# Optimization experiments

Hardware: AMD Instinct MI355X
Metric: run time of the kernel (lower is better)

Reference implementation:

```python
import jax, jax.numpy as jnp
import numpy as np

B, T, H, K = 2048, 200, 256, 8


def setup_inputs() -> dict:
    key = jax.random.key(0)
    ks = jax.random.split(key, 8)
    s = 1.0 / np.sqrt(H)  # torch nn.Linear default init range
    vm = jax.random.uniform(ks[5], (B, T)) < 0.6
    vm = vm.at[:, :3].set(True)  # guarantee >=3 valid visits so history_mask is non-empty
    return {
        "current_state": jax.random.normal(ks[0], (B, H), jnp.float32),
        "state_sequence": jax.random.normal(ks[1], (B, T, H), jnp.float32),
        "visit_mask": vm,
        "Wq": jax.random.uniform(ks[2], (H, H), jnp.float32, -s, s),
        "bq": jnp.zeros((H,), jnp.float32),
        "Wk": jax.random.uniform(ks[3], (H, H), jnp.float32, -s, s),
        "bk": jnp.zeros((H,), jnp.float32),
        "Wv": jax.random.uniform(ks[4], (H, H), jnp.float32, -s, s),
        "bv": jnp.zeros((H,), jnp.float32),
    }


def reference(current_state, state_sequence, visit_mask, Wq, bq, Wk, bk, Wv, bv):
    mask = visit_mask.astype(bool)
    valid_counts = mask.sum(axis=1)  # (B,)
    t_idx = jnp.arange(T)[None, :]
    # attend only to visits strictly before the last valid one
    history_mask = mask & (t_idx < (valid_counts - 1)[:, None])

    q = current_state @ Wq + bq                      # (B,H)
    k = state_sequence @ Wk + bk                     # (B,T,H)
    v = jax.nn.relu(state_sequence @ Wv + bv)        # dropout is identity in eval

    scores = jnp.einsum('bth,bh->bt', k, q) / np.sqrt(H).astype(np.float32)
    scores = jnp.where(history_mask, scores, -1e9)
    attn = jax.nn.softmax(scores, axis=-1)
    attn = jnp.where(history_mask, attn, 0.0)
    norm = attn.sum(-1, keepdims=True)
    attn = attn / jnp.where(norm > 0, norm, 1.0)

    # vectorized per-row top-K sparsify + renormalize (replaces the python loop)
    masked = jnp.where(history_mask, attn, -1.0)
    vals, idx = jax.lax.top_k(masked, K)             # (B,K)
    keep_vals = jnp.maximum(vals, 0.0)               # invalid slots had -1 -> contribute 0
    sparse = jnp.zeros_like(attn).at[jnp.arange(B)[:, None], idx].set(keep_vals)
    eps = jnp.finfo(attn.dtype).eps
    attn = sparse / jnp.maximum(sparse.sum(-1, keepdims=True), eps)

    summary = jnp.einsum('bth,bt->bh', v, attn)
    has_history = history_mask.any(axis=1, keepdims=True)
    summary = jnp.where(has_history, summary, 0.0)

    # selected visit indices (top-K of final weights, -1 where outside history)
    _, midx = jax.lax.top_k(jnp.where(history_mask, attn, -1.0), K)
    sel_mask = jnp.take_along_axis(history_mask, midx, axis=1)
    selected = jnp.where(sel_mask, midx, -1).astype(jnp.int32)

    return summary, attn, selected
```

## Files before the change

### kernel.cpp

```cpp
#include <hip/hip_runtime.h>
#include <cstddef>

#define BB 2048
#define TT 200
#define HH 256
#define KK 8

#define WS_M2T  0
#define WS_EVEC 65792
#define WS_F    66048

__device__ __forceinline__ float wred_sum(float v) {
#pragma unroll
  for (int off = 32; off; off >>= 1) v += __shfl_xor(v, off);
  return v;
}
__device__ __forceinline__ float wred_max(float v) {
#pragma unroll
  for (int off = 32; off; off >>= 1) v = fmaxf(v, __shfl_xor(v, off));
  return v;
}

__global__ __launch_bounds__(256) void prep_all(
    const float* __restrict__ Wq, const float* __restrict__ bq,
    const float* __restrict__ Wk, const float* __restrict__ bk,
    float* __restrict__ M2T, float* __restrict__ evec, float* __restrict__ fsc) {
  const int tid = threadIdx.x;
  __shared__ float As[64][68], Bs[64][68];
  __shared__ float s4[4];
  if (blockIdx.x < 16) {
    const int l0 = ((int)blockIdx.x >> 2) * 64, i0 = ((int)blockIdx.x & 3) * 64;
    const int tl = tid >> 4, ti = tid & 15;
    float acc[4][4];
#pragma unroll
    for (int r = 0; r < 4; ++r)
#pragma unroll
      for (int c = 0; c < 4; ++c) acc[r][c] = 0.f;

    for (int kc = 0; kc < 4; ++kc) {
      const int k0 = kc * 64;
#pragma unroll
      for (int it = 0; it < 4; ++it) {
        int idx = it * 256 + tid;
        int row = idx >> 4, c4 = idx & 15;
        *(float4*)(&As[row][c4 * 4]) =
            *(const float4*)(Wq + (size_t)(l0 + row) * HH + k0 + c4 * 4);
        *(float4*)(&Bs[row][c4 * 4]) =
            *(const float4*)(Wk + (size_t)(i0 + row) * HH + k0 + c4 * 4);
      }
      __syncthreads();
#pragma unroll 4
      for (int k4 = 0; k4 < 16; ++k4) {
        float4 a4[4], b4[4];
#pragma unroll
        for (int r = 0; r < 4; ++r) a4[r] = *(const float4*)(&As[tl * 4 + r][k4 * 4]);
#pragma unroll
        for (int c = 0; c < 4; ++c) b4[c] = *(const float4*)(&Bs[ti * 4 + c][k4 * 4]);
#pragma unroll
        for (int r = 0; r < 4; ++r)
#pragma unroll
          for (int c = 0; c < 4; ++c)
            acc[r][c] += a4[r].x * b4[c].x + a4[r].y * b4[c].y +
                         a4[r].z * b4[c].z + a4[r].w * b4[c].w;
      }
      __syncthreads();
    }
#pragma unroll
    for (int r = 0; r < 4; ++r) {
      float4 o = make_float4(acc[r][0], acc[r][1], acc[r][2], acc[r][3]);
      *(float4*)(M2T + (size_t)(l0 + tl * 4 + r) * HH + i0 + ti * 4) = o;
    }
  } else {
    const int id = (int)blockIdx.x - 16;
    const float* row;
    const float* vec;
    float* outp;
    if (id < 256)      { row = Wk + (size_t)id * HH;         vec = bq; outp = M2T + (size_t)256 * HH + id; }
    else if (id < 512) { row = Wq + (size_t)(id - 256) * HH; vec = bk; outp = evec + (id - 256); }
    else               { row = bk;                           vec = bq; outp = fsc; }
    float p = row[tid] * vec[tid];
    p = wred_sum(p);
    if ((tid & 63) == 0) s4[tid >> 6] = p;
    __syncthreads();
    if (tid == 0) *outp = s4[0] + s4[1] + s4[2] + s4[3];
  }
}

__global__ __launch_bounds__(256, 4) void fused_attn(
    const float* __restrict__ CS, const float* __restrict__ X,
    const int* __restrict__ VM,
    const float* __restrict__ M2T, const float* __restrict__ evec,
    const float* __restrict__ fsc,
    const float* __restrict__ Wv, const float* __restrict__ bvv,
    float* __restrict__ out) {
  const int tid = threadIdx.x, b = blockIdx.x;
  const int w = tid >> 6, lane = tid & 63;
  __shared__ float s_cs[HH];
  __shared__ float s_qk[HH];
  __shared__ float s_part[4][HH];
  __shared__ float s_sc[TT];
  __shared__ float s_cand[256];
  __shared__ int   s_tl[256];
  __shared__ int   s_wc[4];
  __shared__ float s_c4[4], s_r4[4], s_m4[4];
  __shared__ int   s_selI[KK];
  __shared__ float s_selV[KK];
  __shared__ float s_dS;
  __shared__ float s_xg[KK][HH + 4];

  const float csv = CS[(size_t)b * HH + tid];
  s_cs[tid] = csv;
  int m = (tid < TT) ? (VM[(size_t)b * TT + tid] != 0) : 0;
  unsigned long long bal = __ballot(m);
  if (lane == 0) s_c4[w] = (float)__popcll(bal);
  float rq = csv * evec[tid];
  rq = wred_sum(rq);
  if (lane == 0) s_r4[w] = rq;
  __syncthreads();

  const int cnt = (int)(s_c4[0] + s_c4[1] + s_c4[2] + s_c4[3]);
  const int hist_n = cnt - 1;
  const int hist = (m && (tid < hist_n)) ? 1 : 0;
  const float qb = (s_r4[0] + s_r4[1] + s_r4[2] + s_r4[3] + fsc[0]) * 0.0625f;
  const unsigned long long bh = __ballot(hist);
  if (lane == 0) s_wc[w] = __popcll(bh);

  {
    float4 acc4 = make_float4(0.f, 0.f, 0.f, 0.f);
    const int l0 = w * 64;
    const float* mbase = M2T + (size_t)l0 * HH + lane * 4;
#pragma unroll 8
    for (int li = 0; li < 64; ++li) {
      const float a = s_cs[l0 + li];
      const float4 m4 = *(const float4*)(mbase + (size_t)li * HH);
      acc4.x += a * m4.x; acc4.y += a * m4.y;
      acc4.z += a * m4.z; acc4.w += a * m4.w;
    }
    *(float4*)(&s_part[w][lane * 4]) = acc4;
  }
  __syncthreads();
  const int nh = s_wc[0] + s_wc[1] + s_wc[2] + s_wc[3];
  {
    int pre = 0;
#pragma unroll
    for (int i = 0; i < 4; ++i)
      if (i < w) pre += s_wc[i];
    if (hist) s_tl[pre + __popcll(bh & ((1ull << lane) - 1ull))] = tid;

    const float qk = s_part[0][tid] + s_part[1][tid] + s_part[2][tid] +
                     s_part[3][tid] + M2T[(size_t)256 * HH + tid];
    s_qk[tid] = qk * 0.0625f;
  }
  __syncthreads();

  {
    const float* xbase = X + (size_t)b * TT * HH + lane * 4;
    const float4 q4 = ((const float4*)s_qk)[lane];
    int j = w;
    for (; j + 28 < nh; j += 32) {
      int tj[8];
#pragma unroll
      for (int u = 0; u < 8; ++u) tj[u] = s_tl[j + 4 * u];
      float4 xv[8];
#pragma unroll
      for (int u = 0; u < 8; ++u)
        xv[u] = *(const float4*)(xbase + (size_t)tj[u] * HH);
      float pr[8];
#pragma unroll
      for (int u = 0; u < 8; ++u)
        pr[u] = xv[u].x * q4.x + xv[u].y * q4.y + xv[u].z * q4.z + xv[u].w * q4.w;
#pragma unroll
      for (int off = 32; off; off >>= 1)
#pragma unroll
        for (int u = 0; u < 8; ++u) pr[u] += __shfl_xor(pr[u], off);
      if (lane == 0) {
#pragma unroll
        for (int u = 0; u < 8; ++u) s_sc[j + 4 * u] = pr[u] + qb;
      }
    }
    for (; j < nh; j += 4) {
      const int t = s_tl[j];
      float4 xv = *(const float4*)(xbase + (size_t)t * HH);
      float p = xv.x * q4.x + xv.y * q4.y + xv.z * q4.z + xv.w * q4.w;
      p = wred_sum(p);
      if (lane == 0) s_sc[j] = p + qb;
    }
  }
  __syncthreads();

  const int in_l = (tid < nh);
  float v = in_l ? s_sc[tid] : -3.4e38f;
  float wm = wred_max(v);
  if (lane == 0) s_m4[w] = wm;
  __syncthreads();
  const float mx = fmaxf(fmaxf(s_m4[0], s_m4[1]), fmaxf(s_m4[2], s_m4[3]));
  float p = in_l ? expf(v - mx) : 0.f;
  float ws_ = wred_sum(p);
  if (lane == 0) s_r4[w] = ws_;
  __syncthreads();
  const float denom = s_r4[0] + s_r4[1] + s_r4[2] + s_r4[3];
  s_cand[tid] = in_l ? (p / denom) : -2.0f;
  __syncthreads();

  if (tid < 64) {
    float lv[4]; int lt[4];
#pragma unroll
    for (int q = 0; q < 4; ++q) {
      int t = tid + 64 * q;
      lv[q] = s_cand[t];
      lt[q] = t;
    }
    for (int r = 0; r < KK; ++r) {
      float bv = -2.5f; int bi = 1 << 30;
#pragma unroll
      for (int q = 0; q < 4; ++q)
        if (lv[q] > bv) { bv = lv[q]; bi = lt[q]; }
#pragma unroll
      for (int off = 32; off; off >>= 1) {
        float ov = __shfl_xor(bv, off);
        int   oi = __shfl_xor(bi, off);
        if (ov > bv || (ov == bv && oi < bi)) { bv = ov; bi = oi; }
      }
      if (tid == 0) {
        s_selV[r] = bv;
        s_selI[r] = (bv >= 0.f) ? s_tl[bi] : 0;
      }
#pragma unroll
      for (int q = 0; q < 4; ++q)
        if (lt[q] == bi) lv[q] = -3.0f;
    }
    if (tid == 0) {
      float S = 0.f;
#pragma unroll
      for (int r = 0; r < KK; ++r) S += fmaxf(s_selV[r], 0.f);
      s_dS = fmaxf(S, 1.1920929e-07f);
    }
  }
  __syncthreads();

  float* out_attn = out + (size_t)BB * HH + (size_t)b * TT;
  if (tid < TT) out_attn[tid] = 0.f;
#pragma unroll
  for (int it = 0; it < 2; ++it) {
    const int r = it * 4 + (tid >> 6);
    const int t = s_selI[r];
    const int c0 = (tid & 63) * 4;
    *(float4*)(&s_xg[r][c0]) =
        *(const float4*)(X + ((size_t)b * TT + t) * HH + c0);
  }
  __syncthreads();

  if (tid < KK) {
    float vvv = s_selV[tid];
    int   bi  = s_selI[tid];
    float wf  = fmaxf(vvv, 0.f) / s_dS;
    int ok = (vvv >= 0.f);
    if (ok) out_attn[bi] = wf;
    out[(size_t)BB * HH + (size_t)BB * TT + (size_t)b * KK + tid] =
        ok ? (float)bi : -1.0f;
  }

  {
    const int kk = lane >> 4, c16 = lane & 15;
    const float* wvbase = Wv + w * 64 + c16 * 4;
    float4 acc[KK];
#pragma unroll
    for (int r = 0; r < KK; ++r) acc[r] = make_float4(0.f, 0.f, 0.f, 0.f);
#pragma unroll 4
    for (int kb = 0; kb < 64; ++kb) {
      const int k = kb * 4 + kk;
      const float4 wv4 = *(const float4*)(wvbase + (size_t)k * HH);
#pragma unroll
      for (int r = 0; r < KK; ++r) {
        const float xv = s_xg[r][k];
        acc[r].x += xv * wv4.x; acc[r].y += xv * wv4.y;
        acc[r].z += xv * wv4.z; acc[r].w += xv * wv4.w;
      }
    }
#pragma unroll
    for (int r = 0; r < KK; ++r) {
      acc[r].x += __shfl_xor(acc[r].x, 16); acc[r].x += __shfl_xor(acc[r].x, 32);
      acc[r].y += __shfl_xor(acc[r].y, 16); acc[r].y += __shfl_xor(acc[r].y, 32);
      acc[r].z += __shfl_xor(acc[r].z, 16); acc[r].z += __shfl_xor(acc[r].z, 32);
      acc[r].w += __shfl_xor(acc[r].w, 16); acc[r].w += __shfl_xor(acc[r].w, 32);
    }
    if (lane < 16) {
      const float4 bv4 = *(const float4*)(bvv + w * 64 + c16 * 4);
      float4 res = make_float4(0.f, 0.f, 0.f, 0.f);
#pragma unroll
      for (int r = 0; r < KK; ++r) {
        const float wr = fmaxf(s_selV[r], 0.f) / s_dS;
        res.x += wr * fmaxf(acc[r].x + bv4.x, 0.f);
        res.y += wr * fmaxf(acc[r].y + bv4.y, 0.f);
        res.z += wr * fmaxf(acc[r].z + bv4.z, 0.f);
        res.w += wr * fmaxf(acc[r].w + bv4.w, 0.f);
      }
      *(float4*)(out + (size_t)b * HH + w * 64 + c16 * 4) = res;
    }
  }
}

extern "C" void kernel_launch(void* const* d_in, const int* in_sizes, int n_in,
                              void* d_out, int out_size, void* d_ws, size_t ws_size,
                              hipStream_t stream) {
  const float* cs  = (const float*)d_in[0];
  const float* X   = (const float*)d_in[1];
  const int*   vm  = (const int*)d_in[2];
  const float* Wq  = (const float*)d_in[3];
  const float* bq  = (const float*)d_in[4];
  const float* Wk  = (const float*)d_in[5];
  const float* bk  = (const float*)d_in[6];
  const float* Wv  = (const float*)d_in[7];
  const float* bvp = (const float*)d_in[8];
  float* out = (float*)d_out;
  float* ws  = (float*)d_ws;

  float* M2T  = ws + WS_M2T;
  float* evec = ws + WS_EVEC;
  float* fsc  = ws + WS_F;

  hipLaunchKernelGGL(prep_all, dim3(529), dim3(256), 0, stream,
                     Wq, bq, Wk, bk, M2T, evec, fsc);
  hipLaunchKernelGGL(fused_attn, dim3(BB), dim3(256), 0, stream,
                     cs, X, vm, M2T, evec, fsc, Wv, bvp, out);
}
```

Baseline: 563.9 us.

## Process two batch rows per block to reuse M2T and Wv loads

Each block now handles two batch rows, so every M2T row and every Wv row read from global memory feeds two rows' worth of FMAs. The grid is halved to 1024 blocks. The goal is to halve the weight traffic per output row, which dominates the q·M2 and the gathered-value projection. In exchange, shared memory and register pressure (16 float4 accumulators) roughly double, which may cut occupancy below the launch-bounds target, and there are fewer blocks to spread across CUs.

```diff
diff --git a/kernel.cpp b/kernel.cpp
--- a/kernel.cpp
+++ b/kernel.cpp
@@ -86,81 +86,110 @@
   }
 }
 
-__global__ __launch_bounds__(256, 4) void fused_attn(
+__global__ __launch_bounds__(256, 4) void fused_attn2(
     const float* __restrict__ CS, const float* __restrict__ X,
     const int* __restrict__ VM,
     const float* __restrict__ M2T, const float* __restrict__ evec,
     const float* __restrict__ fsc,
     const float* __restrict__ Wv, const float* __restrict__ bvv,
     float* __restrict__ out) {
-  const int tid = threadIdx.x, b = blockIdx.x;
+  const int tid = threadIdx.x;
+  const int b0 = 2 * (int)blockIdx.x, b1 = b0 + 1;
   const int w = tid >> 6, lane = tid & 63;
-  __shared__ float s_cs[HH];
-  __shared__ float s_qk[HH];
-  __shared__ float s_part[4][HH];
-  __shared__ float s_sc[TT];
-  __shared__ float s_cand[256];
-  __shared__ int   s_tl[256];
-  __shared__ int   s_wc[4];
-  __shared__ float s_c4[4], s_r4[4], s_m4[4];
-  __shared__ int   s_selI[KK];
-  __shared__ float s_selV[KK];
-  __shared__ float s_dS;
-  __shared__ float s_xg[KK][HH + 4];
-
-  const float csv = CS[(size_t)b * HH + tid];
-  s_cs[tid] = csv;
-  int m = (tid < TT) ? (VM[(size_t)b * TT + tid] != 0) : 0;
-  unsigned long long bal = __ballot(m);
-  if (lane == 0) s_c4[w] = (float)__popcll(bal);
-  float rq = csv * evec[tid];
-  rq = wred_sum(rq);
-  if (lane == 0) s_r4[w] = rq;
-  __syncthreads();
-
-  const int cnt = (int)(s_c4[0] + s_c4[1] + s_c4[2] + s_c4[3]);
-  const int hist_n = cnt - 1;
-  const int hist = (m && (tid < hist_n)) ? 1 : 0;
-  const float qb = (s_r4[0] + s_r4[1] + s_r4[2] + s_r4[3] + fsc[0]) * 0.0625f;
-  const unsigned long long bh = __ballot(hist);
-  if (lane == 0) s_wc[w] = __popcll(bh);
-
-  {
-    float4 acc4 = make_float4(0.f, 0.f, 0.f, 0.f);
+  __shared__ float s_cs[2][HH];
+  __shared__ float s_qk[2][HH];
+  __shared__ float s_part[4][2][HH];
+  __shared__ float s_sc[2][256];
+  __shared__ float s_cand[2][256];
+  __shared__ int   s_tl[2][256];
+  __shared__ int   s_wc[2][4];
+  __shared__ float s_c4[2][4], s_r4[2][4], s_m4[2][4];
+  __shared__ int   s_selI[2][KK];
+  __shared__ float s_selV[2][KK];
+  __shared__ float s_dS[2];
+  __shared__ float s_xg[2][KK][HH + 4];
+
+  const float csv0 = CS[(size_t)b0 * HH + tid];
+  const float csv1 = CS[(size_t)b1 * HH + tid];
+  s_cs[0][tid] = csv0;
+  s_cs[1][tid] = csv1;
+  const int m0 = (tid < TT) ? (VM[(size_t)b0 * TT + tid] != 0) : 0;
+  const int m1 = (tid < TT) ? (VM[(size_t)b1 * TT + tid] != 0) : 0;
+  {
+    unsigned long long ba0 = __ballot(m0);
+    unsigned long long ba1 = __ballot(m1);
+    if (lane == 0) {
+      s_c4[0][w] = (float)__popcll(ba0);
+      s_c4[1][w] = (float)__popcll(ba1);
+    }
+  }
+  const float ev = evec[tid];
+  {
+    float rq0 = wred_sum(csv0 * ev);
+    float rq1 = wred_sum(csv1 * ev);
+    if (lane == 0) { s_r4[0][w] = rq0; s_r4[1][w] = rq1; }
+  }
+  __syncthreads();
+
+  const int cnt0 = (int)(s_c4[0][0] + s_c4[0][1] + s_c4[0][2] + s_c4[0][3]);
+  const int cnt1 = (int)(s_c4[1][0] + s_c4[1][1] + s_c4[1][2] + s_c4[1][3]);
+  const int hist0 = (m0 && (tid < cnt0 - 1)) ? 1 : 0;
+  const int hist1 = (m1 && (tid < cnt1 - 1)) ? 1 : 0;
+  const float fs = fsc[0];
+  const float qb0 = (s_r4[0][0] + s_r4[0][1] + s_r4[0][2] + s_r4[0][3] + fs) * 0.0625f;
+  const float qb1 = (s_r4[1][0] + s_r4[1][1] + s_r4[1][2] + s_r4[1][3] + fs) * 0.0625f;
+  const unsigned long long bh0 = __ballot(hist0);
+  const unsigned long long bh1 = __ballot(hist1);
+  if (lane == 0) { s_wc[0][w] = __popcll(bh0); s_wc[1][w] = __popcll(bh1); }
+
+  {
+    float4 a0 = make_float4(0.f, 0.f, 0.f, 0.f);
+    float4 a1 = make_float4(0.f, 0.f, 0.f, 0.f);
     const int l0 = w * 64;
     const float* mbase = M2T + (size_t)l0 * HH + lane * 4;
 #pragma unroll 8
     for (int li = 0; li < 64; ++li) {
-      const float a = s_cs[l0 + li];
+      const float c0 = s_cs[0][l0 + li];
+      const float c1 = s_cs[1][l0 + li];
       const float4 m4 = *(const float4*)(mbase + (size_t)li * HH);
-      acc4.x += a * m4.x; acc4.y += a * m4.y;
-      acc4.z += a * m4.z; acc4.w += a * m4.w;
-    }
-    *(float4*)(&s_part[w][lane * 4]) = acc4;
-  }
-  __syncthreads();
-  const int nh = s_wc[0] + s_wc[1] + s_wc[2] + s_wc[3];
-  {
-    int pre = 0;
+      a0.x += c0 * m4.x; a0.y += c0 * m4.y; a0.z += c0 * m4.z; a0.w += c0 * m4.w;
+      a1.x += c1 * m4.x; a1.y += c1 * m4.y; a1.z += c1 * m4.z; a1.w += c1 * m4.w;
+    }
+    *(float4*)(&s_part[w][0][lane * 4]) = a0;
+    *(float4*)(&s_part[w][1][lane * 4]) = a1;
+  }
+  __syncthreads();
+  const int nh0 = s_wc[0][0] + s_wc[0][1] + s_wc[0][2] + s_wc[0][3];
+  const int nh1 = s_wc[1][0] + s_wc[1][1] + s_wc[1][2] + s_wc[1][3];
+  {
+    int pre0 = 0, pre1 = 0;
 #pragma unroll
     for (int i = 0; i < 4; ++i)
-      if (i < w) pre += s_wc[i];
-    if (hist) s_tl[pre + __popcll(bh & ((1ull << lane) - 1ull))] = tid;
-
-    const float qk = s_part[0][tid] + s_part[1][tid] + s_part[2][tid] +
-                     s_part[3][tid] + M2T[(size_t)256 * HH + tid];
-    s_qk[tid] = qk * 0.0625f;
-  }
-  __syncthreads();
-
-  {
-    const float* xbase = X + (size_t)b * TT * HH + lane * 4;
-    const float4 q4 = ((const float4*)s_qk)[lane];
+      if (i < w) { pre0 += s_wc[0][i]; pre1 += s_wc[1][i]; }
+    const unsigned long long below = (1ull << lane) - 1ull;
+    if (hist0) s_tl[0][pre0 + __popcll(bh0 & below)] = tid;
+    if (hist1) s_tl[1][pre1 + __popcll(bh1 & below)] = tid;
+
+    const float dv = M2T[(size_t)256 * HH + tid];
+    s_qk[0][tid] = (s_part[0][0][tid] + s_part[1][0][tid] + s_part[2][0][tid] +
+                    s_part[3][0][tid] + dv) * 0.0625f;
+    s_qk[1][tid] = (s_part[0][1][tid] + s_part[1][1][tid] + s_part[2][1][tid] +
+                    s_part[3][1][tid] + dv) * 0.0625f;
+  }
+  __syncthreads();
+
+#pragma unroll
+  for (int nb = 0; nb < 2; ++nb) {
+    const int bcur = b0 + nb;
+    const int nh = nb ? nh1 : nh0;
+    const float qb = nb ? qb1 : qb0;
+    const float* xbase = X + (size_t)bcur * TT * HH + lane * 4;
+    const float4 q4 = ((const float4*)s_qk[nb])[lane];
     int j = w;
     for (; j + 28 < nh; j += 32) {
       int tj[8];
 #pragma unroll
-      for (int u = 0; u < 8; ++u) tj[u] = s_tl[j + 4 * u];
+      for (int u = 0; u < 8; ++u) tj[u] = s_tl[nb][j + 4 * u];
       float4 xv[8];
 #pragma unroll
       for (int u = 0; u < 8; ++u)
@@ -175,39 +204,51 @@
         for (int u = 0; u < 8; ++u) pr[u] += __shfl_xor(pr[u], off);
       if (lane == 0) {
 #pragma unroll
-        for (int u = 0; u < 8; ++u) s_sc[j + 4 * u] = pr[u] + qb;
+        for (int u = 0; u < 8; ++u) s_sc[nb][j + 4 * u] = pr[u] + qb;
       }
     }
     for (; j < nh; j += 4) {
-      const int t = s_tl[j];
+      const int t = s_tl[nb][j];
       float4 xv = *(const float4*)(xbase + (size_t)t * HH);
       float p = xv.x * q4.x + xv.y * q4.y + xv.z * q4.z + xv.w * q4.w;
       p = wred_sum(p);
-      if (lane == 0) s_sc[j] = p + qb;
-    }
-  }
-  __syncthreads();
-
-  const int in_l = (tid < nh);
-  float v = in_l ? s_sc[tid] : -3.4e38f;
-  float wm = wred_max(v);
-  if (lane == 0) s_m4[w] = wm;
-  __syncthreads();
-  const float mx = fmaxf(fmaxf(s_m4[0], s_m4[1]), fmaxf(s_m4[2], s_m4[3]));
-  float p = in_l ? expf(v - mx) : 0.f;
-  float ws_ = wred_sum(p);
-  if (lane == 0) s_r4[w] = ws_;
-  __syncthreads();
-  const float denom = s_r4[0] + s_r4[1] + s_r4[2] + s_r4[3];
-  s_cand[tid] = in_l ? (p / denom) : -2.0f;
-  __syncthreads();
-
-  if (tid < 64) {
+      if (lane == 0) s_sc[nb][j] = p + qb;
+    }
+  }
+  __syncthreads();
+
+  const int in0 = (tid < nh0), in1 = (tid < nh1);
+  float v0 = in0 ? s_sc[0][tid] : -3.4e38f;
+  float v1 = in1 ? s_sc[1][tid] : -3.4e38f;
+  {
+    float wm0 = wred_max(v0);
+    float wm1 = wred_max(v1);
+    if (lane == 0) { s_m4[0][w] = wm0; s_m4[1][w] = wm1; }
+  }
+  __syncthreads();
+  const float mx0 = fmaxf(fmaxf(s_m4[0][0], s_m4[0][1]), fmaxf(s_m4[0][2], s_m4[0][3]));
+  const float mx1 = fmaxf(fmaxf(s_m4[1][0], s_m4[1][1]), fmaxf(s_m4[1][2], s_m4[1][3]));
+  float p0 = in0 ? expf(v0 - mx0) : 0.f;
+  float p1 = in1 ? expf(v1 - mx1) : 0.f;
+  {
+    float ws0 = wred_sum(p0);
+    float ws1 = wred_sum(p1);
+    if (lane == 0) { s_r4[0][w] = ws0; s_r4[1][w] = ws1; }
+  }
+  __syncthreads();
+  const float den0 = s_r4[0][0] + s_r4[0][1] + s_r4[0][2] + s_r4[0][3];
+  const float den1 = s_r4[1][0] + s_r4[1][1] + s_r4[1][2] + s_r4[1][3];
+  s_cand[0][tid] = in0 ? (p0 / den0) : -2.0f;
+  s_cand[1][tid] = in1 ? (p1 / den1) : -2.0f;
+  __syncthreads();
+
+  if (tid < 128) {
+    const int nb = w;
     float lv[4]; int lt[4];
 #pragma unroll
     for (int q = 0; q < 4; ++q) {
-      int t = tid + 64 * q;
-      lv[q] = s_cand[t];
+      int t = lane + 64 * q;
+      lv[q] = s_cand[nb][t];
       lt[q] = t;
     }
     for (int r = 0; r < KK; ++r) {
@@ -221,81 +262,98 @@
         int   oi = __shfl_xor(bi, off);
         if (ov > bv || (ov == bv && oi < bi)) { bv = ov; bi = oi; }
       }
-      if (tid == 0) {
-        s_selV[r] = bv;
-        s_selI[r] = (bv >= 0.f) ? s_tl[bi] : 0;
+      if (lane == 0) {
+        s_selV[nb][r] = bv;
+        s_selI[nb][r] = (bv >= 0.f) ? s_tl[nb][bi] : 0;
       }
 #pragma unroll
       for (int q = 0; q < 4; ++q)
         if (lt[q] == bi) lv[q] = -3.0f;
     }
-    if (tid == 0) {
+    if (lane == 0) {
       float S = 0.f;
 #pragma unroll
-      for (int r = 0; r < KK; ++r) S += fmaxf(s_selV[r], 0.f);
-      s_dS = fmaxf(S, 1.1920929e-07f);
-    }
-  }
-  __syncthreads();
-
-  float* out_attn = out + (size_t)BB * HH + (size_t)b * TT;
-  if (tid < TT) out_attn[tid] = 0.f;
-#pragma unroll
-  for (int it = 0; it < 2; ++it) {
-    const int r = it * 4 + (tid >> 6);
-    const int t = s_selI[r];
-    const int c0 = (tid & 63) * 4;
-    *(float4*)(&s_xg[r][c0]) =
-        *(const float4*)(X + ((size_t)b * TT + t) * HH + c0);
-  }
-  __syncthreads();
-
-  if (tid < KK) {
-    float vvv = s_selV[tid];
-    int   bi  = s_selI[tid];
-    float wf  = fmaxf(vvv, 0.f) / s_dS;
+      for (int r = 0; r < KK; ++r) S += fmaxf(s_selV[nb][r], 0.f);
+      s_dS[nb] = fmaxf(S, 1.1920929e-07f);
+    }
+  }
+  __syncthreads();
+
+  float* out_attn0 = out + (size_t)BB * HH + (size_t)b0 * TT;
+  float* out_attn1 = out + (size_t)BB * HH + (size_t)b1 * TT;
+  if (tid < TT) { out_attn0[tid] = 0.f; out_attn1[tid] = 0.f; }
+#pragma unroll
+  for (int it = 0; it < 4; ++it) {
+    const int rr = it * 4 + w;
+    const int nb = rr >> 3, r = rr & 7;
+    const int t = s_selI[nb][r];
+    const int c0 = lane * 4;
+    *(float4*)(&s_xg[nb][r][c0]) =
+        *(const float4*)(X + ((size_t)(b0 + nb) * TT + t) * HH + c0);
+  }
+  __syncthreads();
+
+  if (tid < 2 * KK) {
+    const int nb = tid >> 3, r = tid & 7;
+    float vvv = s_selV[nb][r];
+    int   bi  = s_selI[nb][r];
+    float wf  = fmaxf(vvv, 0.f) / s_dS[nb];
     int ok = (vvv >= 0.f);
-    if (ok) out_attn[bi] = wf;
-    out[(size_t)BB * HH + (size_t)BB * TT + (size_t)b * KK + tid] =
+    float* oa = nb ? out_attn1 : out_attn0;
+    if (ok) oa[bi] = wf;
+    out[(size_t)BB * HH + (size_t)BB * TT + (size_t)(b0 + nb) * KK + r] =
         ok ? (float)bi : -1.0f;
   }
 
   {
     const int kk = lane >> 4, c16 = lane & 15;
     const float* wvbase = Wv + w * 64 + c16 * 4;
-    float4 acc[KK];
-#pragma unroll
-    for (int r = 0; r < KK; ++r) acc[r] = make_float4(0.f, 0.f, 0.f, 0.f);
-#pragma unroll 4
+    float4 acc[2][KK];
+#pragma unroll
+    for (int nb = 0; nb < 2; ++nb)
+#pragma unroll
+      for (int r = 0; r < KK; ++r) acc[nb][r] = make_float4(0.f, 0.f, 0.f, 0.f);
+#pragma unroll 2
     for (int kb = 0; kb < 64; ++kb) {
       const int k = kb * 4 + kk;
       const float4 wv4 = *(const float4*)(wvbase + (size_t)k * HH);
 #pragma unroll
+      for (int nb = 0; nb < 2; ++nb)
+#pragma unroll
+        for (int r = 0; r < KK; ++r) {
+          const float xv = s_xg[nb][r][k];
+          acc[nb][r].x += xv * wv4.x; acc[nb][r].y += xv * wv4.y;
+          acc[nb][r].z += xv * wv4.z; acc[nb][r].w += xv * wv4.w;
+        }
+    }
+#pragma unroll
+    for (int nb = 0; nb < 2; ++nb)
+#pragma unroll
       for (int r = 0; r < KK; ++r) {
-        const float xv = s_xg[r][k];
-        acc[r].x += xv * wv4.x; acc[r].y += xv * wv4.y;
-        acc[r].z += xv * wv4.z; acc[r].w += xv * wv4.w;
-      }
-    }
-#pragma unroll
-    for (int r = 0; r < KK; ++r) {
-      acc[r].x += __shfl_xor(acc[r].x, 16); acc[r].x += __shfl_xor(acc[r].x, 32);
-      acc[r].y += __shfl_xor(acc[r].y, 16); acc[r].y += __shfl_xor(acc[r].y, 32);
-      acc[r].z += __shfl_xor(acc[r].z, 16); acc[r].z += __shfl_xor(acc[r].z, 32);
-      acc[r].w += __shfl_xor(acc[r].w, 16); acc[r].w += __shfl_xor(acc[r].w, 32);
-    }
+        acc[nb][r].x += __shfl_xor(acc[nb][r].x, 16);
+        acc[nb][r].x += __shfl_xor(acc[nb][r].x, 32);
+        acc[nb][r].y += __shfl_xor(acc[nb][r].y, 16);
+        acc[nb][r].y += __shfl_xor(acc[nb][r].y, 32);
+        acc[nb][r].z += __shfl_xor(acc[nb][r].z, 16);
+        acc[nb][r].z += __shfl_xor(acc[nb][r].z, 32);
+        acc[nb][r].w += __shfl_xor(acc[nb][r].w, 16);
+        acc[nb][r].w += __shfl_xor(acc[nb][r].w, 32);
+      }
     if (lane < 16) {
       const float4 bv4 = *(const float4*)(bvv + w * 64 + c16 * 4);
-      float4 res = make_float4(0.f, 0.f, 0.f, 0.f);
-#pragma unroll
-      for (int r = 0; r < KK; ++r) {
-        const float wr = fmaxf(s_selV[r], 0.f) / s_dS;
-        res.x += wr * fmaxf(acc[r].x + bv4.x, 0.f);
-        res.y += wr * fmaxf(acc[r].y + bv4.y, 0.f);
-        res.z += wr * fmaxf(acc[r].z + bv4.z, 0.f);
-        res.w += wr * fmaxf(acc[r].w + bv4.w, 0.f);
-      }
-      *(float4*)(out + (size_t)b * HH + w * 64 + c16 * 4) = res;
+#pragma unroll
+      for (int nb = 0; nb < 2; ++nb) {
+        float4 res = make_float4(0.f, 0.f, 0.f, 0.f);
+#pragma unroll
+        for (int r = 0; r < KK; ++r) {
+          const float wr = fmaxf(s_selV[nb][r], 0.f) / s_dS[nb];
+          res.x += wr * fmaxf(acc[nb][r].x + bv4.x, 0.f);
+          res.y += wr * fmaxf(acc[nb][r].y + bv4.y, 0.f);
+          res.z += wr * fmaxf(acc[nb][r].z + bv4.z, 0.f);
+          res.w += wr * fmaxf(acc[nb][r].w + bv4.w, 0.f);
+        }
+        *(float4*)(out + (size_t)(b0 + nb) * HH + w * 64 + c16 * 4) = res;
+      }
     }
   }
 }
@@ -321,6 +379,6 @@
 
   hipLaunchKernelGGL(prep_all, dim3(529), dim3(256), 0, stream,
                      Wq, bq, Wk, bk, M2T, evec, fsc);
-  hipLaunchKernelGGL(fused_attn, dim3(BB), dim3(256), 0, stream,
+  hipLaunchKernelGGL(fused_attn2, dim3(BB / 2), dim3(256), 0, stream,
                      cs, X, vm, M2T, evec, fsc, Wv, bvp, out);
 }
```

Result: no change. 566.9 us (+0.5%).
